# Kernel optimization log

Hardware: AMD Instinct MI355X
Metric: run time of the kernel (lower is better)

The kernel has to match this reference:

```python
import jax, jax.numpy as jnp
import numpy as np

B, T, I, H = 512, 512, 128, 256
EPS = 1e-5


def setup_inputs() -> dict:
    key = jax.random.key(0)
    ks = jax.random.split(key, 8)
    s_ih = 1.0 / np.sqrt(H)
    padded_X = jax.random.normal(ks[0], (B, T, I), dtype=jnp.float32)
    lengths = jax.random.randint(ks[1], (B,), 1, T + 1)  # in [1, T]
    # PyTorch LSTM params: W_ih (4H, I), W_hh (4H, H), biases (4H,), gate order [i,f,g,o]
    W_ih = jax.random.uniform(ks[2], (4 * H, I), minval=-s_ih, maxval=s_ih, dtype=jnp.float32)
    W_hh = jax.random.uniform(ks[3], (4 * H, H), minval=-s_ih, maxval=s_ih, dtype=jnp.float32)
    b_ih = jax.random.uniform(ks[4], (4 * H,), minval=-s_ih, maxval=s_ih, dtype=jnp.float32)
    b_hh = jax.random.uniform(ks[5], (4 * H,), minval=-s_ih, maxval=s_ih, dtype=jnp.float32)
    gamma = jnp.ones((H,), dtype=jnp.float32)
    beta = jnp.zeros((H,), dtype=jnp.float32)
    return {"padded_X": padded_X, "lengths": lengths, "W_ih": W_ih, "W_hh": W_hh,
            "b_ih": b_ih, "b_hh": b_hh, "gamma": gamma, "beta": beta}


def _lstm_last_hidden(padded_X, lengths, W_ih, W_hh, b_ih, b_hh):
    # Precompute input projections for all steps: (B, T, 4H)
    x_proj = jnp.einsum('bti,gi->btg', padded_X, W_ih) + b_ih + b_hh
    x_proj = jnp.swapaxes(x_proj, 0, 1)  # (T, B, 4H)
    ts = jnp.arange(padded_X.shape[1])

    def step(carry, inp):
        h, c = carry
        xp, t = inp
        gates = xp + h @ W_hh.T  # (B, 4H)
        i_g, f_g, g_g, o_g = jnp.split(gates, 4, axis=-1)
        i_g = jax.nn.sigmoid(i_g)
        f_g = jax.nn.sigmoid(f_g)
        g_g = jnp.tanh(g_g)
        o_g = jax.nn.sigmoid(o_g)
        c_new = f_g * c + i_g * g_g
        h_new = o_g * jnp.tanh(c_new)
        # freeze state once past the sequence length (packed-sequence semantics)
        valid = (t < lengths)[:, None]
        h = jnp.where(valid, h_new, h)
        c = jnp.where(valid, c_new, c)
        return (h, c), None

    h0 = jnp.zeros((padded_X.shape[0], W_hh.shape[1]), dtype=padded_X.dtype)
    c0 = jnp.zeros_like(h0)
    (h_fin, _), _ = jax.lax.scan(step, (h0, c0), (x_proj, ts))
    return h_fin  # (B, H) == h_n[-1]


def reference(padded_X, lengths, W_ih, W_hh, b_ih, b_hh, gamma, beta):
    h = _lstm_last_hidden(padded_X, lengths, W_ih, W_hh, b_ih, b_hh)
    mu = jnp.mean(h, axis=-1, keepdims=True)
    var = jnp.mean((h - mu) ** 2, axis=-1, keepdims=True)
    return (h - mu) / jnp.sqrt(var + EPS) * gamma + beta
```

## Files before the change

### kernel.cpp

```cpp
#include <hip/hip_runtime.h>

#define NB 512
#define NT 512
#define NI 128
#define NH 256
#define NG 1024
#define NMT 8
#define NWAVE 8
#define CH 8
#define EPSV 1e-5f

#define WXOFF 32768

typedef short short8 __attribute__((ext_vector_type(8)));
typedef float f32x4 __attribute__((ext_vector_type(4)));

__device__ __forceinline__ unsigned short f32_to_bf16(float f) {
  unsigned int u = __float_as_uint(f);
  u += 0x7fffu + ((u >> 16) & 1u);
  return (unsigned short)(u >> 16);
}
__device__ __forceinline__ float bf16_to_f32(unsigned short u) {
  return __uint_as_float(((unsigned int)u) << 16);
}

__global__ void prep_kernel(const float* __restrict__ W_ih, const float* __restrict__ W_hh,
                            const float* __restrict__ b_ih, const float* __restrict__ b_hh,
                            unsigned short* __restrict__ Wf, float* __restrict__ bsum) {
  int o = blockIdx.x * blockDim.x + threadIdx.x;
  int e = o & 7;
  int l = (o >> 3) & 63;
  int f = o >> 9;
  if (f < 512) {
    int kt = f & 7, m = (f >> 3) & 7, w = f >> 6;
    int row = w * 128 + m * 16 + (l & 15);
    int k = kt * 32 + ((l >> 4) << 3) + e;
    Wf[o] = f32_to_bf16(W_hh[row * NH + k]);
  } else if (f < 768) {
    int g = f - 512;
    int kx = g & 3, m = (g >> 2) & 7, w = g >> 5;
    int row = w * 128 + m * 16 + (l & 15);
    int k = kx * 32 + ((l >> 4) << 3) + e;
    Wf[o] = f32_to_bf16(W_ih[row * NI + k]);
  }
  if (o < NG) bsum[o] = b_ih[o] + b_hh[o];
}

__global__ void sort_kernel(const int* __restrict__ lengths, int* __restrict__ perm) {
  int i = threadIdx.x;
  __shared__ int L[NB];
  int li = lengths[i];
  L[i] = li;
  __syncthreads();
  int r = 0;
  for (int k = 0; k < NB; ++k) {
    int lk = L[k];
    r += (lk > li) || (lk == li && k < i);
  }
  perm[r] = i;
}

__global__ __launch_bounds__(512, 2)
void lstm_ln_kernel(const float* __restrict__ X, const int* __restrict__ lengths,
                    const int* __restrict__ perm,
                    const short8* __restrict__ Wf8, const float* __restrict__ bsum,
                    const float* __restrict__ gamma, const float* __restrict__ beta,
                    float* __restrict__ out) {
  const int p = blockIdx.x;
  const int tid = threadIdx.x;
  const int w = tid >> 6;
  const int l = tid & 63;

  __shared__ short8 ldsW[NWAVE * 14 * 64];
  __shared__ __align__(16) unsigned short gx[2 * CH][NG];
  __shared__ __align__(16) float gh[2][NG];
  __shared__ __align__(16) unsigned short hbuf[2][NH];
  __shared__ float red[20];

  const int b0 = perm[2 * p];
  const int b1 = perm[2 * p + 1];
  const int len0 = lengths[b0];
  const int len1 = lengths[b1];
  const int lmax = (len0 > len1) ? len0 : len1;

  short8 wreg[NMT][5];
#pragma unroll
  for (int m = 0; m < NMT; ++m)
#pragma unroll
    for (int kt = 0; kt < 5; ++kt)
      wreg[m][kt] = Wf8[((w * 8 + m) * 8 + kt) * 64 + l];
  short8 w6a = Wf8[((w * 8 + 6) * 8 + 6) * 64 + l];
  short8 w6b = Wf8[((w * 8 + 7) * 8 + 6) * 64 + l];
#pragma unroll
  for (int m = 0; m < NMT; ++m)
    ldsW[(w * 14 + m) * 64 + l] = Wf8[((w * 8 + m) * 8 + 5) * 64 + l];
#pragma unroll
  for (int m = 0; m < 6; ++m)
    ldsW[(w * 14 + 8 + m) * 64 + l] = Wf8[((w * 8 + m) * 8 + 6) * 64 + l];

  const int s = tid >> 8;
  const int j = tid & 255;
  const int mylen = s ? len1 : len0;
  const float bsi = bsum[j], bsf = bsum[NH + j], bsg = bsum[2 * NH + j], bso = bsum[3 * NH + j];
  float c = 0.f, h = 0.f;

  const float* __restrict__ xr0 = X + (size_t)b0 * NT * NI;
  const float* __restrict__ xr1 = X + (size_t)b1 * NT * NI;
  const int seqb = l & 1;
  const int kg = l >> 4;
  const int st = (l >> 1) & 7;
  const float* __restrict__ xp = seqb ? xr1 : xr0;

  hbuf[s][j] = 0;
  __syncthreads();

  for (int t = 0; t < lmax; ++t) {
    if ((t & 7) == 0) {
      const float* xb = xp + (size_t)(t + st) * NI + kg * 8;
      const int cc = l & 15;
#pragma unroll
      for (int half = 0; half < 2; ++half) {
        f32x4 ax[4];
#pragma unroll
        for (int m = 0; m < 4; ++m) ax[m] = (f32x4){0.f, 0.f, 0.f, 0.f};
#pragma unroll
        for (int kx = 0; kx < 4; ++kx) {
          float4 xa = *(const float4*)(xb + kx * 32);
          float4 xc = *(const float4*)(xb + kx * 32 + 4);
          short8 bx;
          bx[0] = (short)f32_to_bf16(xa.x); bx[1] = (short)f32_to_bf16(xa.y);
          bx[2] = (short)f32_to_bf16(xa.z); bx[3] = (short)f32_to_bf16(xa.w);
          bx[4] = (short)f32_to_bf16(xc.x); bx[5] = (short)f32_to_bf16(xc.y);
          bx[6] = (short)f32_to_bf16(xc.z); bx[7] = (short)f32_to_bf16(xc.w);
#pragma unroll
          for (int m = 0; m < 4; ++m) {
            short8 wi = Wf8[WXOFF + ((w * 8 + half * 4 + m) * 4 + kx) * 64 + l];
            ax[m] = __builtin_amdgcn_mfma_f32_16x16x32_bf16(wi, bx, ax[m], 0, 0, 0);
          }
        }
#pragma unroll
        for (int m = 0; m < 4; ++m) {
          int r0 = w * 128 + (half * 4 + m) * 16 + kg * 4;
          ushort4 pk;
          pk.x = f32_to_bf16(ax[m][0]); pk.y = f32_to_bf16(ax[m][1]);
          pk.z = f32_to_bf16(ax[m][2]); pk.w = f32_to_bf16(ax[m][3]);
          *(ushort4*)&gx[cc][r0] = pk;
        }
      }
    }

    f32x4 acc[NMT];
#pragma unroll
    for (int m = 0; m < NMT; ++m) acc[m] = (f32x4){0.f, 0.f, 0.f, 0.f};

#pragma unroll
    for (int kt = 0; kt < 5; ++kt) {
      short8 bh = *(const short8*)&hbuf[seqb][kt * 32 + kg * 8];
#pragma unroll
      for (int m = 0; m < NMT; ++m)
        acc[m] = __builtin_amdgcn_mfma_f32_16x16x32_bf16(wreg[m][kt], bh, acc[m], 0, 0, 0);
    }
    short8 sw[NMT];
#pragma unroll
    for (int m = 0; m < 4; ++m)
      sw[m] = Wf8[((w * 8 + m) * 8 + 7) * 64 + l];
    {
      short8 bh = *(const short8*)&hbuf[seqb][5 * 32 + kg * 8];
#pragma unroll
      for (int m = 0; m < NMT; ++m)
        acc[m] = __builtin_amdgcn_mfma_f32_16x16x32_bf16(ldsW[(w * 14 + m) * 64 + l], bh,
                                                         acc[m], 0, 0, 0);
    }
    short8 bh7 = *(const short8*)&hbuf[seqb][7 * 32 + kg * 8];
#pragma unroll
    for (int m = 0; m < 4; ++m)
      acc[m] = __builtin_amdgcn_mfma_f32_16x16x32_bf16(sw[m], bh7, acc[m], 0, 0, 0);
#pragma unroll
    for (int m = 4; m < 8; ++m)
      sw[m] = Wf8[((w * 8 + m) * 8 + 7) * 64 + l];
    {
      short8 bh = *(const short8*)&hbuf[seqb][6 * 32 + kg * 8];
#pragma unroll
      for (int m = 0; m < 6; ++m)
        acc[m] = __builtin_amdgcn_mfma_f32_16x16x32_bf16(ldsW[(w * 14 + 8 + m) * 64 + l], bh,
                                                         acc[m], 0, 0, 0);
      acc[6] = __builtin_amdgcn_mfma_f32_16x16x32_bf16(w6a, bh, acc[6], 0, 0, 0);
      acc[7] = __builtin_amdgcn_mfma_f32_16x16x32_bf16(w6b, bh, acc[7], 0, 0, 0);
    }
#pragma unroll
    for (int m = 4; m < 8; ++m)
      acc[m] = __builtin_amdgcn_mfma_f32_16x16x32_bf16(sw[m], bh7, acc[m], 0, 0, 0);

    if ((l & 15) < 2) {
#pragma unroll
      for (int m = 0; m < NMT; ++m)
        *(f32x4*)&gh[l & 1][w * 128 + m * 16 + kg * 4] = acc[m];
    }
    __syncthreads();

    {
      const int dt = ((t & 7) << 1) + s;
      float pi = gh[s][j]          + bf16_to_f32(gx[dt][j])          + bsi;
      float pf = gh[s][NH + j]     + bf16_to_f32(gx[dt][NH + j])     + bsf;
      float pg = gh[s][2 * NH + j] + bf16_to_f32(gx[dt][2 * NH + j]) + bsg;
      float po = gh[s][3 * NH + j] + bf16_to_f32(gx[dt][3 * NH + j]) + bso;
      if (t < mylen) {
        float ig = 1.f / (1.f + __expf(-pi));
        float fg = 1.f / (1.f + __expf(-pf));
        float gv = 1.f - 2.f / (1.f + __expf(2.f * pg));
        float og = 1.f / (1.f + __expf(-po));
        c = fg * c + ig * gv;
        h = og * (1.f - 2.f / (1.f + __expf(2.f * c)));
        hbuf[s][j] = f32_to_bf16(h);
      }
    }
    __syncthreads();
  }

  float sum = h, sq = h * h;
#pragma unroll
  for (int off = 32; off > 0; off >>= 1) {
    sum += __shfl_xor(sum, off);
    sq  += __shfl_xor(sq, off);
  }
  if (l == 0) { red[w] = sum; red[8 + w] = sq; }
  __syncthreads();
  if (tid == 0) {
    float S = red[0] + red[1] + red[2] + red[3];
    float Q = red[8] + red[9] + red[10] + red[11];
    float mu = S * (1.f / NH);
    red[16] = mu;
    red[17] = rsqrtf(Q * (1.f / NH) - mu * mu + EPSV);
  }
  if (tid == 256) {
    float S = red[4] + red[5] + red[6] + red[7];
    float Q = red[12] + red[13] + red[14] + red[15];
    float mu = S * (1.f / NH);
    red[18] = mu;
    red[19] = rsqrtf(Q * (1.f / NH) - mu * mu + EPSV);
  }
  __syncthreads();
  {
    float mu = red[16 + 2 * s], rstd = red[17 + 2 * s];
    int b = s ? b1 : b0;
    out[(size_t)b * NH + j] = (h - mu) * rstd * gamma[j] + beta[j];
  }
}

extern "C" void kernel_launch(void* const* d_in, const int* in_sizes, int n_in,
                              void* d_out, int out_size, void* d_ws, size_t ws_size,
                              hipStream_t stream) {
  const float* X       = (const float*)d_in[0];
  const int*   lengths = (const int*)d_in[1];
  const float* W_ih    = (const float*)d_in[2];
  const float* W_hh    = (const float*)d_in[3];
  const float* b_ih    = (const float*)d_in[4];
  const float* b_hh    = (const float*)d_in[5];
  const float* gamma   = (const float*)d_in[6];
  const float* beta    = (const float*)d_in[7];
  float* out = (float*)d_out;

  unsigned short* Wf = (unsigned short*)d_ws;
  float* bsum = (float*)((char*)d_ws + (size_t)768 * 512 * sizeof(unsigned short));
  int* perm = (int*)((char*)bsum + NG * sizeof(float));

  int total = 768 * 512;
  prep_kernel<<<(total + 255) / 256, 256, 0, stream>>>(W_ih, W_hh, b_ih, b_hh, Wf, bsum);
  sort_kernel<<<1, NB, 0, stream>>>(lengths, perm);
  lstm_ln_kernel<<<NB / 2, 512, 0, stream>>>(X, lengths, perm, (const short8*)Wf, bsum,
                                             gamma, beta, out);
}
```

Before: 2.699 ms.

## Precompute input projection in separate GEMM kernel and stream it into recurrence

Adds a separate GEMM kernel that computes the bf16 input projection plus bias for all batch rows and timesteps into a large workspace buffer. The recurrent kernel then streams each step's precomputed gates into LDS with async global-to-LDS loads, staged three steps ahead, instead of computing the x-projection chunk by chunk inside the serial loop. This takes the input MFMA work off the latency-bound recurrence, at the cost of a 512 MB workspace round trip and an extra launch. The old fused path is kept as a fallback when the workspace is too small.

```diff
diff --git a/kernel.cpp b/kernel.cpp
--- a/kernel.cpp
+++ b/kernel.cpp
@@ -7,10 +7,10 @@
 #define NG 1024
 #define NMT 8
 #define NWAVE 8
-#define CH 8
 #define EPSV 1e-5f
 
 #define WXOFF 32768
+#define GXOFF_BYTES (1u << 20)
 
 typedef short short8 __attribute__((ext_vector_type(8)));
 typedef float f32x4 __attribute__((ext_vector_type(4)));
@@ -22,6 +22,11 @@
 }
 __device__ __forceinline__ float bf16_to_f32(unsigned short u) {
   return __uint_as_float(((unsigned int)u) << 16);
+}
+__device__ __forceinline__ void gload_lds16(const void* g, void* l) {
+  __builtin_amdgcn_global_load_lds(
+      (const __attribute__((address_space(1))) unsigned int*)g,
+      (__attribute__((address_space(3))) unsigned int*)l, 16, 0, 0);
 }
 
 __global__ void prep_kernel(const float* __restrict__ W_ih, const float* __restrict__ W_hh,
@@ -61,18 +66,228 @@
 }
 
 __global__ __launch_bounds__(512, 2)
-void lstm_ln_kernel(const float* __restrict__ X, const int* __restrict__ lengths,
-                    const int* __restrict__ perm,
-                    const short8* __restrict__ Wf8, const float* __restrict__ bsum,
-                    const float* __restrict__ gamma, const float* __restrict__ beta,
-                    float* __restrict__ out) {
+void gemm_xproj(const float* __restrict__ X, const short8* __restrict__ Wf8,
+                const float* __restrict__ bsum, unsigned short* __restrict__ gxall) {
+  const int b = blockIdx.y;
+  const int t0 = blockIdx.x * 64;
+  const int tid = threadIdx.x;
+  const int w = tid >> 6, l = tid & 63;
+  __shared__ __align__(16) unsigned short tile[16][1032];
+
+  short8 wi[NMT][4];
+#pragma unroll
+  for (int m = 0; m < NMT; ++m)
+#pragma unroll
+    for (int kx = 0; kx < 4; ++kx)
+      wi[m][kx] = Wf8[WXOFF + ((w * 8 + m) * 4 + kx) * 64 + l];
+
+  const int c = l & 15, kg = l >> 4;
+  for (int nt = 0; nt < 4; ++nt) {
+    const float* xrow = X + ((size_t)b * NT + t0 + nt * 16 + c) * NI + kg * 8;
+    f32x4 acc[NMT];
+#pragma unroll
+    for (int m = 0; m < NMT; ++m) acc[m] = (f32x4){0.f, 0.f, 0.f, 0.f};
+#pragma unroll
+    for (int kx = 0; kx < 4; ++kx) {
+      float4 xa = *(const float4*)(xrow + kx * 32);
+      float4 xc = *(const float4*)(xrow + kx * 32 + 4);
+      short8 bx;
+      bx[0] = (short)f32_to_bf16(xa.x); bx[1] = (short)f32_to_bf16(xa.y);
+      bx[2] = (short)f32_to_bf16(xa.z); bx[3] = (short)f32_to_bf16(xa.w);
+      bx[4] = (short)f32_to_bf16(xc.x); bx[5] = (short)f32_to_bf16(xc.y);
+      bx[6] = (short)f32_to_bf16(xc.z); bx[7] = (short)f32_to_bf16(xc.w);
+#pragma unroll
+      for (int m = 0; m < NMT; ++m)
+        acc[m] = __builtin_amdgcn_mfma_f32_16x16x32_bf16(wi[m][kx], bx, acc[m], 0, 0, 0);
+    }
+#pragma unroll
+    for (int m = 0; m < NMT; ++m) {
+      int rb = w * 128 + m * 16 + kg * 4;
+      f32x4 bv = *(const f32x4*)&bsum[rb];
+      ushort4 pk;
+      pk.x = f32_to_bf16(acc[m][0] + bv[0]); pk.y = f32_to_bf16(acc[m][1] + bv[1]);
+      pk.z = f32_to_bf16(acc[m][2] + bv[2]); pk.w = f32_to_bf16(acc[m][3] + bv[3]);
+      *(ushort4*)&tile[c][rb] = pk;
+    }
+    __syncthreads();
+    {
+      unsigned short* dst = gxall + ((size_t)b * NT + t0 + nt * 16) * NG;
+#pragma unroll
+      for (int rep = 0; rep < 4; ++rep) {
+        int r = (tid >> 7) + rep * 4;
+        int col = (tid & 127) * 8;
+        *(uint4*)&dst[(size_t)r * NG + col] = *(const uint4*)&tile[r][col];
+      }
+    }
+    __syncthreads();
+  }
+}
+
+__global__ __launch_bounds__(512, 2)
+void lstm_ln_pre(const int* __restrict__ lengths, const int* __restrict__ perm,
+                 const short8* __restrict__ Wf8, const unsigned short* __restrict__ gxall,
+                 const float* __restrict__ gamma, const float* __restrict__ beta,
+                 float* __restrict__ out) {
   const int p = blockIdx.x;
   const int tid = threadIdx.x;
   const int w = tid >> 6;
   const int l = tid & 63;
 
+  __shared__ short8 ldsW[NWAVE * 16 * 64];
+  __shared__ __align__(16) unsigned short gstage[4][2][NG];
+  __shared__ __align__(16) float gh[2][NG];
+  __shared__ __align__(16) unsigned short hbuf[2][NH];
+  __shared__ float red[20];
+
+  const int b0 = perm[2 * p];
+  const int b1 = perm[2 * p + 1];
+  const int len0 = lengths[b0];
+  const int len1 = lengths[b1];
+  const int lmax = (len0 > len1) ? len0 : len1;
+
+  short8 wreg[NMT][5];
+#pragma unroll
+  for (int m = 0; m < NMT; ++m)
+#pragma unroll
+    for (int kt = 0; kt < 5; ++kt)
+      wreg[m][kt] = Wf8[((w * 8 + m) * 8 + kt) * 64 + l];
+#pragma unroll
+  for (int m = 0; m < NMT; ++m) {
+    ldsW[(w * 16 + m) * 64 + l]     = Wf8[((w * 8 + m) * 8 + 5) * 64 + l];
+    ldsW[(w * 16 + 8 + m) * 64 + l] = Wf8[((w * 8 + m) * 8 + 6) * 64 + l];
+  }
+
+  const int s = tid >> 8;
+  const int j = tid & 255;
+  const int mylen = s ? len1 : len0;
+  float c = 0.f, h = 0.f;
+  hbuf[s][j] = 0;
+
+  auto stage = [&](int t2) {
+    if (w < 4) {
+      int t2c = (t2 < NT) ? t2 : NT - 1;
+      const unsigned short* gp = gxall
+          + ((size_t)(w >= 2 ? b1 : b0) * NT + t2c) * NG + (w & 1) * 512 + (size_t)l * 8;
+      gload_lds16(gp, &gstage[t2 & 3][w >> 1][(w & 1) * 512]);
+    }
+  };
+  stage(0); stage(1); stage(2);
+  __syncthreads();
+
+  const int seqb = l & 1;
+  const int kg = l >> 4;
+
+  for (int t = 0; t < lmax; ++t) {
+    stage(t + 3);
+
+    f32x4 acc[NMT];
+#pragma unroll
+    for (int m = 0; m < NMT; ++m) acc[m] = (f32x4){0.f, 0.f, 0.f, 0.f};
+
+#pragma unroll
+    for (int kt = 0; kt < 5; ++kt) {
+      short8 bh = *(const short8*)&hbuf[seqb][kt * 32 + kg * 8];
+#pragma unroll
+      for (int m = 0; m < NMT; ++m)
+        acc[m] = __builtin_amdgcn_mfma_f32_16x16x32_bf16(wreg[m][kt], bh, acc[m], 0, 0, 0);
+    }
+    short8 swA[4];
+#pragma unroll
+    for (int m = 0; m < 4; ++m) swA[m] = Wf8[((w * 8 + m) * 8 + 7) * 64 + l];
+    {
+      short8 bh = *(const short8*)&hbuf[seqb][5 * 32 + kg * 8];
+#pragma unroll
+      for (int m = 0; m < NMT; ++m)
+        acc[m] = __builtin_amdgcn_mfma_f32_16x16x32_bf16(ldsW[(w * 16 + m) * 64 + l], bh,
+                                                         acc[m], 0, 0, 0);
+    }
+    short8 bh7 = *(const short8*)&hbuf[seqb][7 * 32 + kg * 8];
+#pragma unroll
+    for (int m = 0; m < 4; ++m)
+      acc[m] = __builtin_amdgcn_mfma_f32_16x16x32_bf16(swA[m], bh7, acc[m], 0, 0, 0);
+    short8 swB[4];
+#pragma unroll
+    for (int m = 0; m < 4; ++m) swB[m] = Wf8[((w * 8 + 4 + m) * 8 + 7) * 64 + l];
+    {
+      short8 bh = *(const short8*)&hbuf[seqb][6 * 32 + kg * 8];
+#pragma unroll
+      for (int m = 0; m < NMT; ++m)
+        acc[m] = __builtin_amdgcn_mfma_f32_16x16x32_bf16(ldsW[(w * 16 + 8 + m) * 64 + l], bh,
+                                                         acc[m], 0, 0, 0);
+    }
+#pragma unroll
+    for (int m = 0; m < 4; ++m)
+      acc[4 + m] = __builtin_amdgcn_mfma_f32_16x16x32_bf16(swB[m], bh7, acc[4 + m], 0, 0, 0);
+
+    if ((l & 15) < 2) {
+#pragma unroll
+      for (int m = 0; m < NMT; ++m)
+        *(f32x4*)&gh[l & 1][w * 128 + m * 16 + kg * 4] = acc[m];
+    }
+    __syncthreads();
+
+    {
+      const unsigned short* gs = &gstage[t & 3][s][0];
+      float pi = gh[s][j]          + bf16_to_f32(gs[j]);
+      float pf = gh[s][NH + j]     + bf16_to_f32(gs[NH + j]);
+      float pg = gh[s][2 * NH + j] + bf16_to_f32(gs[2 * NH + j]);
+      float po = gh[s][3 * NH + j] + bf16_to_f32(gs[3 * NH + j]);
+      if (t < mylen) {
+        float ig = 1.f / (1.f + __expf(-pi));
+        float fg = 1.f / (1.f + __expf(-pf));
+        float gv = 1.f - 2.f / (1.f + __expf(2.f * pg));
+        float og = 1.f / (1.f + __expf(-po));
+        c = fg * c + ig * gv;
+        h = og * (1.f - 2.f / (1.f + __expf(2.f * c)));
+        hbuf[s][j] = f32_to_bf16(h);
+      }
+    }
+    __syncthreads();
+  }
+
+  float sum = h, sq = h * h;
+#pragma unroll
+  for (int off = 32; off > 0; off >>= 1) {
+    sum += __shfl_xor(sum, off);
+    sq  += __shfl_xor(sq, off);
+  }
+  if (l == 0) { red[w] = sum; red[8 + w] = sq; }
+  __syncthreads();
+  if (tid == 0) {
+    float S = red[0] + red[1] + red[2] + red[3];
+    float Q = red[8] + red[9] + red[10] + red[11];
+    float mu = S * (1.f / NH);
+    red[16] = mu;
+    red[17] = rsqrtf(Q * (1.f / NH) - mu * mu + EPSV);
+  }
+  if (tid == 256) {
+    float S = red[4] + red[5] + red[6] + red[7];
+    float Q = red[12] + red[13] + red[14] + red[15];
+    float mu = S * (1.f / NH);
+    red[18] = mu;
+    red[19] = rsqrtf(Q * (1.f / NH) - mu * mu + EPSV);
+  }
+  __syncthreads();
+  {
+    float mu = red[16 + 2 * s], rstd = red[17 + 2 * s];
+    int b = s ? b1 : b0;
+    out[(size_t)b * NH + j] = (h - mu) * rstd * gamma[j] + beta[j];
+  }
+}
+
+__global__ __launch_bounds__(512, 2)
+void lstm_ln_chunk(const float* __restrict__ X, const int* __restrict__ lengths,
+                   const int* __restrict__ perm,
+                   const short8* __restrict__ Wf8, const float* __restrict__ bsum,
+                   const float* __restrict__ gamma, const float* __restrict__ beta,
+                   float* __restrict__ out) {
+  const int p = blockIdx.x;
+  const int tid = threadIdx.x;
+  const int w = tid >> 6;
+  const int l = tid & 63;
+
   __shared__ short8 ldsW[NWAVE * 14 * 64];
-  __shared__ __align__(16) unsigned short gx[2 * CH][NG];
+  __shared__ __align__(16) unsigned short gx[16][NG];
   __shared__ __align__(16) float gh[2][NG];
   __shared__ __align__(16) unsigned short hbuf[2][NH];
   __shared__ float red[20];
@@ -152,7 +367,6 @@
     f32x4 acc[NMT];
 #pragma unroll
     for (int m = 0; m < NMT; ++m) acc[m] = (f32x4){0.f, 0.f, 0.f, 0.f};
-
 #pragma unroll
     for (int kt = 0; kt < 5; ++kt) {
       short8 bh = *(const short8*)&hbuf[seqb][kt * 32 + kg * 8];
@@ -263,10 +477,19 @@
   unsigned short* Wf = (unsigned short*)d_ws;
   float* bsum = (float*)((char*)d_ws + (size_t)768 * 512 * sizeof(unsigned short));
   int* perm = (int*)((char*)bsum + NG * sizeof(float));
+  unsigned short* gxall = (unsigned short*)((char*)d_ws + GXOFF_BYTES);
 
   int total = 768 * 512;
   prep_kernel<<<(total + 255) / 256, 256, 0, stream>>>(W_ih, W_hh, b_ih, b_hh, Wf, bsum);
   sort_kernel<<<1, NB, 0, stream>>>(lengths, perm);
-  lstm_ln_kernel<<<NB / 2, 512, 0, stream>>>(X, lengths, perm, (const short8*)Wf, bsum,
-                                             gamma, beta, out);
-}
+
+  size_t need = (size_t)GXOFF_BYTES + (size_t)NB * NT * NG * sizeof(unsigned short);
+  if (ws_size >= need) {
+    gemm_xproj<<<dim3(NT / 64, NB), 512, 0, stream>>>(X, (const short8*)Wf, bsum, gxall);
+    lstm_ln_pre<<<NB / 2, 512, 0, stream>>>(lengths, perm, (const short8*)Wf, gxall,
+                                            gamma, beta, out);
+  } else {
+    lstm_ln_chunk<<<NB / 2, 512, 0, stream>>>(X, lengths, perm, (const short8*)Wf, bsum,
+                                              gamma, beta, out);
+  }
+}
```

Result: no change. 2.699 ms (+0.0%).
